# Kernel optimization log

Measured on AMD Instinct MI355X. Metric: run time of the kernel, lower is better.

## Reference

```python
import jax, jax.numpy as jnp
import numpy as np

N = 2048
D = 512
E = 65536
THR = 0.0          # config['edge_threshold']
CLUSTER_RANGE = 2
NEG_SLOPE = 0.01   # F.leaky_relu default


def segment_softmax(x, seg, num_segments):
    # torch_geometric.utils.softmax over segments (here: source nodes)
    m = jax.ops.segment_max(x, seg, num_segments)
    e = jnp.exp(x - m[seg])
    s = jax.ops.segment_sum(e, seg, num_segments)
    return e / (s[seg] + 1e-16)


def setup_inputs() -> dict:
    key = jax.random.key(0)
    k1, k2, k3 = jax.random.split(key, 3)
    embedding = jax.random.normal(k1, (N, D), dtype=jnp.float32)
    edge_index = jax.random.randint(k2, (2, E), 0, N)
    src, dst = edge_index[0], edge_index[1]
    edge_matrix = jnp.zeros((N, N), jnp.float32).at[src, dst].set(1.0)
    edge_matrix_weight = edge_matrix  # unit edge weights
    W_score = (jax.random.normal(k3, (2 * D, 1), dtype=jnp.float32) / np.sqrt(2.0 * D)).astype(jnp.float32)
    b_score = jnp.zeros((1,), jnp.float32)
    return {"embedding": embedding, "edge_index": edge_index,
            "edge_matrix": edge_matrix, "edge_matrix_weight": edge_matrix_weight,
            "W_score": W_score, "b_score": b_score}


def reference(embedding, edge_index, edge_matrix, edge_matrix_weight, W_score, b_score):
    n = embedding.shape[0]
    dt = embedding.dtype
    diag = jnp.eye(n, dtype=bool)

    # connectivity fitness: Z @ Z.T with L2-normalized rows
    Z = embedding / jnp.maximum(jnp.linalg.norm(embedding, axis=-1, keepdims=True), 1e-12)
    connectivity_M = Z @ Z.T                                   # [N,N]

    # structural fitness: edge-score -> leaky_relu -> segment softmax -> dense scatter
    src, dst = edge_index[0], edge_index[1]
    x_pair = jnp.concatenate([embedding[src], embedding[dst]], axis=-1) @ W_score + b_score  # [E,1]
    x_score = jax.nn.leaky_relu(x_pair[:, 0], NEG_SLOPE)
    x_score = segment_softmax(x_score, src, n)
    structure_M = jnp.zeros((n, n), dt).at[src, dst].add(x_score)
    fitness = connectivity_M + structure_M                     # fitness_mode == 'both_j'

    # Generate_clusters (cluster_range = 2)
    mat = jnp.where(diag, 0.0, edge_matrix)
    mat = jnp.where(fitness < THR, 0.0, mat)
    A1 = mat
    A2 = (jnp.where(diag, 0.0, A1 @ A1) > 0.5).astype(dt)
    A2 = jnp.maximum(A2 - A1, 0.0)
    cluster_matrix = ((A1 + A2) > 0).astype(dt)

    # Cluster_assignment: mean fitness per cluster matrix, nan -> 0
    scores = jnp.zeros((n,), dt)
    for A in (A1, A2):
        deg = A.sum(-1)
        scores = scores + jnp.where(deg > 0, (fitness * A).sum(-1) / jnp.where(deg > 0, deg, 1.0), 0.0)
    cluster_scores = scores / CLUSTER_RANGE

    # Select_clusters (overlap=True, pick_all=True): local extrema over A1 neighborhood
    local_extrema = (cluster_scores[:, None] - A1 * cluster_scores[None, :]) > 0
    is_cluster = local_extrema.all(axis=-1)                    # boolean cluster-center mask

    # Generate_assignment_matrix (mask-based instead of column slicing; removed
    # 'reduced' columns are kept as zero columns so shapes stay static)
    S = cluster_matrix
    S_f = cluster_matrix * fitness
    reduced = (S * is_cluster.astype(dt)[None, :]).sum(-1) > 0   # member of a selected cluster
    isolated = S.sum(0) == 0
    reduced = reduced | isolated
    keeping = (~is_cluster) & (~reduced)

    S = jnp.where(keeping[None, :], 0.0, S)
    S_f = jnp.where(keeping[None, :], 0.0, S_f)
    S = jnp.where(diag, 1.0, S)
    S_f = jnp.where(diag, 1.0, S_f)
    col_keep = (~reduced).astype(dt)[None, :]
    S = S * col_keep
    S_f = S_f * col_keep

    # pooling_mode == 'mean': pooled embedding = S_w.T @ X
    pooled = S_f.T @ embedding                                  # [N, D], zero rows = removed nodes
    return pooled
```

## Files before the change

kernel.cpp:

```cpp
#include <hip/hip_runtime.h>
#include <cstdint>
#include <cstddef>

typedef unsigned long long u64;
typedef unsigned int u32;
typedef _Float16 half8 __attribute__((ext_vector_type(8)));
typedef float f32x4 __attribute__((ext_vector_type(4)));

#define NN 2048
#define DD 512
#define EE 65536
#define NW 32

__global__ __launch_bounds__(256) void k_node(const float* __restrict__ emb,
                                              const float* __restrict__ Wsc,
                                              float* inv_norm, float* av, float* cv,
                                              _Float16* __restrict__ zh,
                                              _Float16* __restrict__ zl,
                                              float* ssum,
                                              u64* centerBits, u64* colAny, u64* EBw) {
    int n = blockIdx.x;
    int t = threadIdx.x;
    if (n < 256) EBw[n * 256 + t] = 0ull;
    else if (n < 264) { int idx = (n - 256) * 256 + t; ssum[idx] = 0.0f; }
    else if (n == 264 && t < NW) { centerBits[t] = 0ull; colAny[t] = 0ull; }

    const float* row = emb + (size_t)n * DD;
    float ss = 0.f, aa = 0.f, cc = 0.f;
    for (int d = t; d < DD; d += 256) {
        float v = row[d];
        ss += v * v;
        aa += v * Wsc[d];
        cc += v * Wsc[DD + d];
    }
    for (int off = 32; off; off >>= 1) {
        ss += __shfl_down(ss, off);
        aa += __shfl_down(aa, off);
        cc += __shfl_down(cc, off);
    }
    __shared__ float red[3][4];
    __shared__ float s_inv;
    int wid = t >> 6, lane = t & 63;
    if (lane == 0) { red[0][wid] = ss; red[1][wid] = aa; red[2][wid] = cc; }
    __syncthreads();
    if (t == 0) {
        float s = 0.f, a = 0.f, c = 0.f;
        for (int w = 0; w < 4; w++) { s += red[0][w]; a += red[1][w]; c += red[2][w]; }
        float iv = 1.0f / fmaxf(sqrtf(s), 1e-12f);
        inv_norm[n] = iv;
        s_inv = iv;
        av[n] = a;
        cv[n] = c;
    }
    __syncthreads();
    float iv = s_inv;
    for (int d = t; d < DD; d += 256) {
        float z = row[d] * iv;
        _Float16 h = (_Float16)z;
        _Float16 l = (_Float16)(z - (float)h);
        zh[(size_t)n * DD + d] = h;
        zl[(size_t)n * DD + d] = l;
    }
}

__device__ __forceinline__ float edge_score(const int* ei, const float* av, const float* cv,
                                            float b0, int e, int* src, int* dst) {
    int s = ei[e], d = ei[EE + e];
    *src = s; *dst = d;
    float x = av[s] + cv[d] + b0;
    return x > 0.f ? x : 0.01f * x;
}

__global__ __launch_bounds__(256) void k_edgeA(const int* __restrict__ ei,
                                               const float* __restrict__ av,
                                               const float* __restrict__ cv,
                                               const float* __restrict__ bsc,
                                               float* ssum, u64* EBw) {
    int e = blockIdx.x * 256 + threadIdx.x;
    if (e >= EE) return;
    int s, d;
    float x = edge_score(ei, av, cv, bsc[0], e, &s, &d);
    atomicAdd(&ssum[s], expf(x));
    atomicOr(&EBw[(size_t)s * NW + (d >> 6)], 1ull << (d & 63));
}

__global__ __launch_bounds__(256) void k_edge_scatter(const int* __restrict__ ei,
                                                      const float* __restrict__ av,
                                                      const float* __restrict__ cv,
                                                      const float* __restrict__ bsc,
                                                      const float* __restrict__ ssum,
                                                      float* fit) {
    int e = blockIdx.x * 256 + threadIdx.x;
    if (e >= EE) return;
    int s, d;
    float x = edge_score(ei, av, cv, bsc[0], e, &s, &d);
    float w = expf(x) / (ssum[s] + 1e-16f);
    atomicAdd(&fit[(size_t)s * NN + d], w);
}

#define BK 64
__global__ __launch_bounds__(256) void k_fitness(const _Float16* __restrict__ zh,
                                                 const _Float16* __restrict__ zl,
                                                 float* __restrict__ fit) {
    __shared__ _Float16 SM[4 * 64 * BK];
    _Float16* Ah = SM;
    _Float16* Al = SM + 64 * BK;
    _Float16* Bh = SM + 2 * 64 * BK;
    _Float16* Bl = SM + 3 * 64 * BK;
    int tid = threadIdx.x;
    int wid = tid >> 6, lane = tid & 63;
    int wr = wid >> 1, wc = wid & 1;
    int p = blockIdx.x, bi = 0;
    while (p >= 32 - bi) { p -= 32 - bi; bi++; }
    int bj = bi + p;
    int I = bi * 64, J = bj * 64;
    int lr = lane & 15;
    int q = lane >> 4;
    f32x4 acc[2][2] = {};

    int rl0 = tid >> 3, sl0 = tid & 7;
    int rl1 = (256 + tid) >> 3, sl1 = tid & 7;
    int ks0 = ((sl0 ^ (rl0 & 7)) << 3);
    int ks1 = ((sl1 ^ (rl1 & 7)) << 3);
    size_t gA0 = (size_t)(I + rl0) * DD + ks0, gB0 = (size_t)(J + rl0) * DD + ks0;
    size_t gA1 = (size_t)(I + rl1) * DD + ks1, gB1 = (size_t)(J + rl1) * DD + ks1;
    int lo0 = rl0 * BK + sl0 * 8, lo1 = rl1 * BK + sl1 * 8;

    {
        half8 a0 = *reinterpret_cast<const half8*>(&zh[gA0]);
        half8 a1 = *reinterpret_cast<const half8*>(&zh[gA1]);
        half8 l0 = *reinterpret_cast<const half8*>(&zl[gA0]);
        half8 l1 = *reinterpret_cast<const half8*>(&zl[gA1]);
        half8 b0 = *reinterpret_cast<const half8*>(&zh[gB0]);
        half8 b1 = *reinterpret_cast<const half8*>(&zh[gB1]);
        half8 m0 = *reinterpret_cast<const half8*>(&zl[gB0]);
        half8 m1 = *reinterpret_cast<const half8*>(&zl[gB1]);
        *reinterpret_cast<half8*>(&Ah[lo0]) = a0;
        *reinterpret_cast<half8*>(&Ah[lo1]) = a1;
        *reinterpret_cast<half8*>(&Al[lo0]) = l0;
        *reinterpret_cast<half8*>(&Al[lo1]) = l1;
        *reinterpret_cast<half8*>(&Bh[lo0]) = b0;
        *reinterpret_cast<half8*>(&Bh[lo1]) = b1;
        *reinterpret_cast<half8*>(&Bl[lo0]) = m0;
        *reinterpret_cast<half8*>(&Bl[lo1]) = m1;
    }
    __syncthreads();

    for (int k0 = 0; k0 < DD; k0 += BK) {
        half8 nA0, nA1, nAl0, nAl1, nB0, nB1, nBl0, nBl1;
        bool hasNext = (k0 + BK) < DD;
        if (hasNext) {
            int kn = k0 + BK;
            nA0  = *reinterpret_cast<const half8*>(&zh[gA0 + kn]);
            nA1  = *reinterpret_cast<const half8*>(&zh[gA1 + kn]);
            nAl0 = *reinterpret_cast<const half8*>(&zl[gA0 + kn]);
            nAl1 = *reinterpret_cast<const half8*>(&zl[gA1 + kn]);
            nB0  = *reinterpret_cast<const half8*>(&zh[gB0 + kn]);
            nB1  = *reinterpret_cast<const half8*>(&zh[gB1 + kn]);
            nBl0 = *reinterpret_cast<const half8*>(&zl[gB0 + kn]);
            nBl1 = *reinterpret_cast<const half8*>(&zl[gB1 + kn]);
        }
#pragma unroll
        for (int kk = 0; kk < 2; kk++) {
            half8 a_h[2], a_l[2], b_h[2], b_l[2];
#pragma unroll
            for (int f = 0; f < 2; f++) {
                int ra = wr * 32 + f * 16 + lr;
                int ca = (kk * 4 + q) ^ (ra & 7);
                int oa = ra * BK + ca * 8;
                a_h[f] = *reinterpret_cast<const half8*>(&Ah[oa]);
                a_l[f] = *reinterpret_cast<const half8*>(&Al[oa]);
                int rb = wc * 32 + f * 16 + lr;
                int cb = (kk * 4 + q) ^ (rb & 7);
                int ob = rb * BK + cb * 8;
                b_h[f] = *reinterpret_cast<const half8*>(&Bh[ob]);
                b_l[f] = *reinterpret_cast<const half8*>(&Bl[ob]);
            }
#pragma unroll
            for (int u = 0; u < 2; u++)
#pragma unroll
                for (int v = 0; v < 2; v++) {
                    acc[u][v] = __builtin_amdgcn_mfma_f32_16x16x32_f16(a_h[u], b_h[v], acc[u][v], 0, 0, 0);
                    acc[u][v] = __builtin_amdgcn_mfma_f32_16x16x32_f16(a_h[u], b_l[v], acc[u][v], 0, 0, 0);
                    acc[u][v] = __builtin_amdgcn_mfma_f32_16x16x32_f16(a_l[u], b_h[v], acc[u][v], 0, 0, 0);
                }
        }
        if (hasNext) {
            __syncthreads();
            *reinterpret_cast<half8*>(&Ah[lo0]) = nA0;
            *reinterpret_cast<half8*>(&Ah[lo1]) = nA1;
            *reinterpret_cast<half8*>(&Al[lo0]) = nAl0;
            *reinterpret_cast<half8*>(&Al[lo1]) = nAl1;
            *reinterpret_cast<half8*>(&Bh[lo0]) = nB0;
            *reinterpret_cast<half8*>(&Bh[lo1]) = nB1;
            *reinterpret_cast<half8*>(&Bl[lo0]) = nBl0;
            *reinterpret_cast<half8*>(&Bl[lo1]) = nBl1;
            __syncthreads();
        }
    }
#pragma unroll
    for (int u = 0; u < 2; u++) {
        int r = I + wr * 32 + u * 16 + q * 4;
#pragma unroll
        for (int v = 0; v < 2; v++) {
            int c = J + wc * 32 + v * 16 + lr;
#pragma unroll
            for (int i2 = 0; i2 < 4; i2++)
                fit[(size_t)(r + i2) * NN + c] = acc[u][v][i2];
        }
    }
    if (bi != bj) {
        __syncthreads();
        float* Tw = reinterpret_cast<float*>(SM) + wid * 528;
#pragma unroll
        for (int v = 0; v < 2; v++) {
#pragma unroll
            for (int u = 0; u < 2; u++)
#pragma unroll
                for (int i2 = 0; i2 < 4; i2++)
                    Tw[lr * 33 + u * 16 + q * 4 + i2] = acc[u][v][i2];
            int cbase = J + wc * 32 + v * 16;
            int rbase = I + wr * 32;
#pragma unroll
            for (int rr = 0; rr < 8; rr++) {
                int row = rr * 2 + (lane >> 5);
                int col = lane & 31;
                fit[(size_t)(cbase + row) * NN + rbase + col] = Tw[row * 33 + col];
            }
        }
    }
}

__global__ void k_bits(const u64* __restrict__ EBw, const float* __restrict__ fit,
                       u64* __restrict__ A1w) {
    int i = blockIdx.x;
    int t = threadIdx.x;
    int lane = t & 63, wv = t >> 6;
    for (int q = 0; q < 8; q++) {
        int j = q * 256 + t;
        u64 eb = EBw[(size_t)i * NW + (j >> 6)];
        float f = fit[(size_t)i * NN + j];
        bool pred = ((eb >> (j & 63)) & 1) && (j != i) && (f >= 0.f);
        u64 word = __ballot(pred);
        if (lane == 0) A1w[i * NW + q * 4 + wv] = word;
    }
}

__global__ __launch_bounds__(256) void k_paths2s(const u64* __restrict__ A1w,
                                                 const float* __restrict__ fit,
                                                 u64* __restrict__ A2w, u64* __restrict__ CLw,
                                                 float* cs) {
    int i = blockIdx.x;
    __shared__ u64 rowA[NW];
    __shared__ u64 rowA2[NW];
    __shared__ u64 part[8][NW];
    int t = threadIdx.x;
    if (t < NW) rowA[t] = A1w[i * NW + t];
    __syncthreads();
    int g = t >> 5, w = t & 31;
    u64 acc = 0;
    for (int ww = 0; ww < 4; ww++) {
        u64 bits = rowA[g * 4 + ww];
        int kbase = (g * 4 + ww) * 64;
        while (bits) {
            int k = __ffsll((unsigned long long)bits) - 1;
            bits &= bits - 1;
            acc |= A1w[(size_t)(kbase + k) * NW + w];
        }
    }
    part[g][w] = acc;
    __syncthreads();
    if (g == 0) {
        u64 p2 = part[0][w];
#pragma unroll
        for (int gg = 1; gg < 8; gg++) p2 |= part[gg][w];
        if ((i >> 6) == w) p2 &= ~(1ull << (i & 63));
        u64 a1 = rowA[w];
        u64 a2 = p2 & ~a1;
        u64 cl = a1 | a2;
        A2w[i * NW + w] = a2;
        CLw[i * NW + w] = cl;
        rowA2[w] = a2;
    }
    __syncthreads();
    float s1 = 0.f, s2 = 0.f;
    int d1 = 0, d2 = 0;
    for (int q = 0; q < 8; q++) {
        int j = q * 256 + t;
        float f = fit[(size_t)i * NN + j];
        int ww = j >> 6, b = j & 63;
        u64 a1 = rowA[ww], a2 = rowA2[ww];
        if ((a1 >> b) & 1) { s1 += f; d1++; }
        if ((a2 >> b) & 1) { s2 += f; d2++; }
    }
    for (int off = 32; off; off >>= 1) {
        s1 += __shfl_down(s1, off);
        s2 += __shfl_down(s2, off);
        d1 += __shfl_down(d1, off);
        d2 += __shfl_down(d2, off);
    }
    __shared__ float rs1[4], rs2[4];
    __shared__ int rd1[4], rd2[4];
    int wid = t >> 6, lane = t & 63;
    if (lane == 0) { rs1[wid] = s1; rs2[wid] = s2; rd1[wid] = d1; rd2[wid] = d2; }
    __syncthreads();
    if (t == 0) {
        float S1 = 0.f, S2 = 0.f; int D1 = 0, D2 = 0;
        for (int w2 = 0; w2 < 4; w2++) { S1 += rs1[w2]; S2 += rs2[w2]; D1 += rd1[w2]; D2 += rd2[w2]; }
        float v1 = D1 > 0 ? S1 / (float)D1 : 0.f;
        float v2 = D2 > 0 ? S2 / (float)D2 : 0.f;
        cs[i] = 0.5f * (v1 + v2);
    }
}

__global__ __launch_bounds__(256) void k_extcol(const u64* __restrict__ A1w,
                                                const u64* __restrict__ CLw,
                                                const float* __restrict__ cs,
                                                unsigned char* is_c, u64* centerBits,
                                                u64* colAny) {
    int i = blockIdx.x, t = threadIdx.x;
    __shared__ u64 part[8][NW];
    if (i < 64) {
        int sub = t >> 5, w = t & 31;
        u64 acc = 0;
#pragma unroll
        for (int k = 0; k < 4; k++) {
            int r = i * 32 + sub + k * 8;
            acc |= CLw[(size_t)r * NW + w];
        }
        part[sub][w] = acc;
    }
    float ci = cs[i];
    int ok = 1;
    for (int q = 0; q < 8; q++) {
        int j = q * 256 + t;
        u64 a1 = A1w[i * NW + (j >> 6)];
        float other = ((a1 >> (j & 63)) & 1) ? cs[j] : 0.0f;
        ok &= ((ci - other) > 0.0f) ? 1 : 0;
    }
    int all = __syncthreads_and(ok);
    if (t == 0) {
        is_c[i] = (unsigned char)(all ? 1 : 0);
        if (all) atomicOr(&centerBits[i >> 6], 1ull << (i & 63));
    }
    if (i < 64 && t < NW) {
        u64 v = part[0][t];
#pragma unroll
        for (int s = 1; s < 8; s++) v |= part[s][t];
        atomicOr(&colAny[t], v);
    }
}

__global__ __launch_bounds__(256) void k_pooled(const float* __restrict__ fit,
                                                const float* __restrict__ emb,
                                                const u64* __restrict__ CLw,
                                                const u64* __restrict__ centerBits,
                                                const u64* __restrict__ colAny,
                                                const unsigned char* __restrict__ is_c,
                                                float* __restrict__ out) {
    int j = blockIdx.x;
    int t = threadIdx.x;
    bool red = ((colAny[j >> 6] >> (j & 63)) & 1ull) == 0ull;
    for (int w = 0; w < NW; w++) red |= (CLw[(size_t)j * NW + w] & centerBits[w]) != 0ull;
    const float2* embj = reinterpret_cast<const float2*>(emb + (size_t)j * DD);
    float2* outj = reinterpret_cast<float2*>(out + (size_t)j * DD);
    bool active = is_c[j] && !red;
    if (!active) {
        float dg = red ? 0.0f : 1.0f;
        float2 v = embj[t];
        float2 o; o.x = v.x * dg; o.y = v.y * dg;
        outj[t] = o;
        return;
    }
    __shared__ int lidx[NN];
    __shared__ float lwt[NN];
    __shared__ int wcnt[4];
    int wid = t >> 6, lane = t & 63;
    int wsh = j >> 6;
    u64 bmask = 1ull << (j & 63);
    int total = 0;
    for (int qq = 0; qq < 8; qq++) {
        int i = qq * 256 + t;
        u64 cw = CLw[(size_t)i * NW + wsh];
        bool p = (cw & bmask) != 0ull;
        float f = 0.f;
        if (p) f = fit[(size_t)i * NN + j];
        u64 mask = __ballot(p);
        if (lane == 0) wcnt[wid] = __popcll(mask);
        __syncthreads();
        int off = total;
        for (int w = 0; w < wid; w++) off += wcnt[w];
        int tq = wcnt[0] + wcnt[1] + wcnt[2] + wcnt[3];
        if (p) {
            int pos = off + __popcll(mask & ((1ull << lane) - 1ull));
            lidx[pos] = i;
            lwt[pos] = f;
        }
        total += tq;
        __syncthreads();
    }
    float2 acc = {0.f, 0.f};
    int k = 0;
    for (; k + 16 <= total; k += 16) {
        int idxr[16];
        float wtr[16];
#pragma unroll
        for (int u = 0; u < 16; u++) { idxr[u] = lidx[k + u]; wtr[u] = lwt[k + u]; }
        float2 e[16];
#pragma unroll
        for (int u = 0; u < 16; u++)
            e[u] = reinterpret_cast<const float2*>(emb + (size_t)idxr[u] * DD)[t];
#pragma unroll
        for (int u = 0; u < 16; u++) {
            acc.x += wtr[u] * e[u].x;
            acc.y += wtr[u] * e[u].y;
        }
    }
    for (; k < total; k++) {
        int i = lidx[k];
        float w = lwt[k];
        float2 e = reinterpret_cast<const float2*>(emb + (size_t)i * DD)[t];
        acc.x += w * e.x;
        acc.y += w * e.y;
    }
    float2 v = embj[t];
    acc.x += v.x;
    acc.y += v.y;
    outj[t] = acc;
}

extern "C" void kernel_launch(void* const* d_in, const int* in_sizes, int n_in,
                              void* d_out, int out_size, void* d_ws, size_t ws_size,
                              hipStream_t stream) {
    const float* emb = (const float*)d_in[0];
    const int*   ei  = (const int*)d_in[1];
    const float* Wsc = (const float*)d_in[4];
    const float* bsc = (const float*)d_in[5];
    float* out = (float*)d_out;

    char* ws = (char*)d_ws;
    size_t off = 0;
    auto alloc = [&](size_t bytes) -> char* {
        char* p = ws + off;
        off = (off + bytes + 255) & ~(size_t)255;
        return p;
    };
    float* fit  = (float*)alloc((size_t)NN * NN * 4);
    char*  zblk = alloc((size_t)2 * NN * DD * 2);
    _Float16* zh = (_Float16*)zblk;
    _Float16* zl = (_Float16*)(zblk + (size_t)NN * DD * 2);
    u64* A1w = (u64*)zblk;
    u64* A2w = (u64*)(zblk + (size_t)NN * NW * 8);
    u64* CLw = (u64*)(zblk + (size_t)2 * NN * NW * 8);
    u64*   EBw        = (u64*)alloc((size_t)NN * NW * 8);
    u64*   centerBits = (u64*)alloc(NW * 8);
    u64*   colAny     = (u64*)alloc(NW * 8);
    float* inv_norm   = (float*)alloc(NN * 4);
    float* av         = (float*)alloc(NN * 4);
    float* cv         = (float*)alloc(NN * 4);
    float* ssum       = (float*)alloc(NN * 4);
    float* cs         = (float*)alloc(NN * 4);
    unsigned char* is_c = (unsigned char*)alloc(NN);

    k_node<<<dim3(NN), dim3(256), 0, stream>>>(emb, Wsc, inv_norm, av, cv, zh, zl,
                                               ssum, centerBits, colAny, EBw);
    k_edgeA<<<dim3(EE / 256), dim3(256), 0, stream>>>(ei, av, cv, bsc, ssum, EBw);
    k_fitness<<<dim3(528), dim3(256), 0, stream>>>(zh, zl, fit);
    k_edge_scatter<<<dim3(EE / 256), dim3(256), 0, stream>>>(ei, av, cv, bsc, ssum, fit);
    k_bits<<<dim3(NN), dim3(256), 0, stream>>>(EBw, fit, A1w);
    k_paths2s<<<dim3(NN), dim3(256), 0, stream>>>(A1w, fit, A2w, CLw, cs);
    k_extcol<<<dim3(NN), dim3(256), 0, stream>>>(A1w, CLw, cs, is_c, centerBits, colAny);
    k_pooled<<<dim3(NN), dim3(256), 0, stream>>>(fit, emb, CLw, centerBits, colAny, is_c, out);
}
```

Before: 146.2 us.

## Fuse all pipeline stages into one cooperative persistent kernel with grid syncs

Replaces the eight separate kernel launches with a single cooperative kernel that walks through each stage using grid-stride loops and separates dependent stages with grid.sync(). The workspace is also re-laid out so zh/zl no longer alias the bit matrices. The aim is to remove per-launch overhead and the idle gaps between small dependent kernels. In exchange, the grid is capped at 1024 blocks, so parallelism in the node and pooling stages drops, grid-wide barriers add their own cost, and occupancy is limited by the 32KB shared buffer and launch bounds.

```diff
diff --git a/kernel.cpp b/kernel.cpp
--- a/kernel.cpp
+++ b/kernel.cpp
@@ -1,6 +1,9 @@
 #include <hip/hip_runtime.h>
+#include <hip/hip_cooperative_groups.h>
 #include <cstdint>
 #include <cstddef>
+
+namespace cg = cooperative_groups;
 
 typedef unsigned long long u64;
 typedef unsigned int u32;
@@ -11,422 +14,364 @@
 #define DD 512
 #define EE 65536
 #define NW 32
-
-__global__ __launch_bounds__(256) void k_node(const float* __restrict__ emb,
-                                              const float* __restrict__ Wsc,
-                                              float* inv_norm, float* av, float* cv,
-                                              _Float16* __restrict__ zh,
-                                              _Float16* __restrict__ zl,
-                                              float* ssum,
-                                              u64* centerBits, u64* colAny, u64* EBw) {
-    int n = blockIdx.x;
-    int t = threadIdx.x;
-    if (n < 256) EBw[n * 256 + t] = 0ull;
-    else if (n < 264) { int idx = (n - 256) * 256 + t; ssum[idx] = 0.0f; }
-    else if (n == 264 && t < NW) { centerBits[t] = 0ull; colAny[t] = 0ull; }
-
-    const float* row = emb + (size_t)n * DD;
-    float ss = 0.f, aa = 0.f, cc = 0.f;
-    for (int d = t; d < DD; d += 256) {
-        float v = row[d];
-        ss += v * v;
-        aa += v * Wsc[d];
-        cc += v * Wsc[DD + d];
-    }
-    for (int off = 32; off; off >>= 1) {
-        ss += __shfl_down(ss, off);
-        aa += __shfl_down(aa, off);
-        cc += __shfl_down(cc, off);
-    }
-    __shared__ float red[3][4];
-    __shared__ float s_inv;
-    int wid = t >> 6, lane = t & 63;
-    if (lane == 0) { red[0][wid] = ss; red[1][wid] = aa; red[2][wid] = cc; }
-    __syncthreads();
-    if (t == 0) {
-        float s = 0.f, a = 0.f, c = 0.f;
-        for (int w = 0; w < 4; w++) { s += red[0][w]; a += red[1][w]; c += red[2][w]; }
-        float iv = 1.0f / fmaxf(sqrtf(s), 1e-12f);
-        inv_norm[n] = iv;
-        s_inv = iv;
-        av[n] = a;
-        cv[n] = c;
-    }
-    __syncthreads();
-    float iv = s_inv;
-    for (int d = t; d < DD; d += 256) {
-        float z = row[d] * iv;
-        _Float16 h = (_Float16)z;
-        _Float16 l = (_Float16)(z - (float)h);
-        zh[(size_t)n * DD + d] = h;
-        zl[(size_t)n * DD + d] = l;
-    }
-}
-
-__device__ __forceinline__ float edge_score(const int* ei, const float* av, const float* cv,
-                                            float b0, int e, int* src, int* dst) {
-    int s = ei[e], d = ei[EE + e];
-    *src = s; *dst = d;
-    float x = av[s] + cv[d] + b0;
-    return x > 0.f ? x : 0.01f * x;
-}
-
-__global__ __launch_bounds__(256) void k_edgeA(const int* __restrict__ ei,
-                                               const float* __restrict__ av,
-                                               const float* __restrict__ cv,
-                                               const float* __restrict__ bsc,
-                                               float* ssum, u64* EBw) {
-    int e = blockIdx.x * 256 + threadIdx.x;
-    if (e >= EE) return;
-    int s, d;
-    float x = edge_score(ei, av, cv, bsc[0], e, &s, &d);
-    atomicAdd(&ssum[s], expf(x));
-    atomicOr(&EBw[(size_t)s * NW + (d >> 6)], 1ull << (d & 63));
-}
-
-__global__ __launch_bounds__(256) void k_edge_scatter(const int* __restrict__ ei,
-                                                      const float* __restrict__ av,
-                                                      const float* __restrict__ cv,
-                                                      const float* __restrict__ bsc,
-                                                      const float* __restrict__ ssum,
-                                                      float* fit) {
-    int e = blockIdx.x * 256 + threadIdx.x;
-    if (e >= EE) return;
-    int s, d;
-    float x = edge_score(ei, av, cv, bsc[0], e, &s, &d);
-    float w = expf(x) / (ssum[s] + 1e-16f);
-    atomicAdd(&fit[(size_t)s * NN + d], w);
-}
-
 #define BK 64
-__global__ __launch_bounds__(256) void k_fitness(const _Float16* __restrict__ zh,
-                                                 const _Float16* __restrict__ zl,
-                                                 float* __restrict__ fit) {
-    __shared__ _Float16 SM[4 * 64 * BK];
-    _Float16* Ah = SM;
-    _Float16* Al = SM + 64 * BK;
-    _Float16* Bh = SM + 2 * 64 * BK;
-    _Float16* Bl = SM + 3 * 64 * BK;
-    int tid = threadIdx.x;
-    int wid = tid >> 6, lane = tid & 63;
-    int wr = wid >> 1, wc = wid & 1;
-    int p = blockIdx.x, bi = 0;
-    while (p >= 32 - bi) { p -= 32 - bi; bi++; }
-    int bj = bi + p;
-    int I = bi * 64, J = bj * 64;
-    int lr = lane & 15;
-    int q = lane >> 4;
-    f32x4 acc[2][2] = {};
-
-    int rl0 = tid >> 3, sl0 = tid & 7;
-    int rl1 = (256 + tid) >> 3, sl1 = tid & 7;
-    int ks0 = ((sl0 ^ (rl0 & 7)) << 3);
-    int ks1 = ((sl1 ^ (rl1 & 7)) << 3);
-    size_t gA0 = (size_t)(I + rl0) * DD + ks0, gB0 = (size_t)(J + rl0) * DD + ks0;
-    size_t gA1 = (size_t)(I + rl1) * DD + ks1, gB1 = (size_t)(J + rl1) * DD + ks1;
-    int lo0 = rl0 * BK + sl0 * 8, lo1 = rl1 * BK + sl1 * 8;
-
-    {
-        half8 a0 = *reinterpret_cast<const half8*>(&zh[gA0]);
-        half8 a1 = *reinterpret_cast<const half8*>(&zh[gA1]);
-        half8 l0 = *reinterpret_cast<const half8*>(&zl[gA0]);
-        half8 l1 = *reinterpret_cast<const half8*>(&zl[gA1]);
-        half8 b0 = *reinterpret_cast<const half8*>(&zh[gB0]);
-        half8 b1 = *reinterpret_cast<const half8*>(&zh[gB1]);
-        half8 m0 = *reinterpret_cast<const half8*>(&zl[gB0]);
-        half8 m1 = *reinterpret_cast<const half8*>(&zl[gB1]);
-        *reinterpret_cast<half8*>(&Ah[lo0]) = a0;
-        *reinterpret_cast<half8*>(&Ah[lo1]) = a1;
-        *reinterpret_cast<half8*>(&Al[lo0]) = l0;
-        *reinterpret_cast<half8*>(&Al[lo1]) = l1;
-        *reinterpret_cast<half8*>(&Bh[lo0]) = b0;
-        *reinterpret_cast<half8*>(&Bh[lo1]) = b1;
-        *reinterpret_cast<half8*>(&Bl[lo0]) = m0;
-        *reinterpret_cast<half8*>(&Bl[lo1]) = m1;
-    }
-    __syncthreads();
-
-    for (int k0 = 0; k0 < DD; k0 += BK) {
-        half8 nA0, nA1, nAl0, nAl1, nB0, nB1, nBl0, nBl1;
-        bool hasNext = (k0 + BK) < DD;
-        if (hasNext) {
-            int kn = k0 + BK;
-            nA0  = *reinterpret_cast<const half8*>(&zh[gA0 + kn]);
-            nA1  = *reinterpret_cast<const half8*>(&zh[gA1 + kn]);
-            nAl0 = *reinterpret_cast<const half8*>(&zl[gA0 + kn]);
-            nAl1 = *reinterpret_cast<const half8*>(&zl[gA1 + kn]);
-            nB0  = *reinterpret_cast<const half8*>(&zh[gB0 + kn]);
-            nB1  = *reinterpret_cast<const half8*>(&zh[gB1 + kn]);
-            nBl0 = *reinterpret_cast<const half8*>(&zl[gB0 + kn]);
-            nBl1 = *reinterpret_cast<const half8*>(&zl[gB1 + kn]);
-        }
-#pragma unroll
-        for (int kk = 0; kk < 2; kk++) {
-            half8 a_h[2], a_l[2], b_h[2], b_l[2];
-#pragma unroll
-            for (int f = 0; f < 2; f++) {
-                int ra = wr * 32 + f * 16 + lr;
-                int ca = (kk * 4 + q) ^ (ra & 7);
-                int oa = ra * BK + ca * 8;
-                a_h[f] = *reinterpret_cast<const half8*>(&Ah[oa]);
-                a_l[f] = *reinterpret_cast<const half8*>(&Al[oa]);
-                int rb = wc * 32 + f * 16 + lr;
-                int cb = (kk * 4 + q) ^ (rb & 7);
-                int ob = rb * BK + cb * 8;
-                b_h[f] = *reinterpret_cast<const half8*>(&Bh[ob]);
-                b_l[f] = *reinterpret_cast<const half8*>(&Bl[ob]);
-            }
-#pragma unroll
-            for (int u = 0; u < 2; u++)
+
+__device__ __forceinline__ float leaky(float x) { return x > 0.f ? x : 0.01f * x; }
+
+__global__ __launch_bounds__(256, 4) void k_mega(
+    const float* __restrict__ emb, const int* __restrict__ ei,
+    const float* __restrict__ Wsc, const float* __restrict__ bsc,
+    float* __restrict__ out,
+    float* __restrict__ fit, _Float16* __restrict__ zh, _Float16* __restrict__ zl,
+    u64* __restrict__ A1w, u64* __restrict__ A2w, u64* __restrict__ CLw,
+    u64* __restrict__ EBw, u64* centerBits, u64* colAny,
+    float* ssum, float* cs, float* av, float* cv, unsigned char* is_c)
+{
+    cg::grid_group grid = cg::this_grid();
+    __shared__ alignas(16) char SMEM[32768];
+    const int b = blockIdx.x, t = threadIdx.x, G = gridDim.x;
+    const int wid = t >> 6, lane = t & 63;
+
+    for (int idx = b * 256 + t; idx < NN * NW; idx += G * 256) EBw[idx] = 0ull;
+    for (int idx = b * 256 + t; idx < NN; idx += G * 256) ssum[idx] = 0.f;
+    if (b == 0 && t < NW) { centerBits[t] = 0ull; colAny[t] = 0ull; }
+    {
+        float* red = (float*)SMEM;
+        float* s_inv = (float*)(SMEM + 64);
+        for (int n = b; n < NN; n += G) {
+            const float* row = emb + (size_t)n * DD;
+            float ss = 0.f, aa = 0.f, cc = 0.f;
+            for (int d = t; d < DD; d += 256) {
+                float v = row[d];
+                ss += v * v; aa += v * Wsc[d]; cc += v * Wsc[DD + d];
+            }
+            for (int off = 32; off; off >>= 1) {
+                ss += __shfl_down(ss, off);
+                aa += __shfl_down(aa, off);
+                cc += __shfl_down(cc, off);
+            }
+            if (lane == 0) { red[wid] = ss; red[4 + wid] = aa; red[8 + wid] = cc; }
+            __syncthreads();
+            if (t == 0) {
+                float s = 0, a = 0, c = 0;
+                for (int w = 0; w < 4; w++) { s += red[w]; a += red[4 + w]; c += red[8 + w]; }
+                *s_inv = 1.0f / fmaxf(sqrtf(s), 1e-12f);
+                av[n] = a; cv[n] = c;
+            }
+            __syncthreads();
+            float iv = *s_inv;
+            for (int d = t; d < DD; d += 256) {
+                float z = row[d] * iv;
+                _Float16 h = (_Float16)z;
+                _Float16 l = (_Float16)(z - (float)h);
+                zh[(size_t)n * DD + d] = h;
+                zl[(size_t)n * DD + d] = l;
+            }
+            __syncthreads();
+        }
+    }
+    grid.sync();
+
+    {
+        _Float16* Ah = (_Float16*)SMEM;
+        _Float16* Al = Ah + 64 * BK;
+        _Float16* Bh = Ah + 2 * 64 * BK;
+        _Float16* Bl = Ah + 3 * 64 * BK;
+        int wr = wid >> 1, wc = wid & 1;
+        int lr = lane & 15, q = lane >> 4;
+        int rl0 = t >> 3, sl0 = t & 7;
+        int rl1 = (256 + t) >> 3, sl1 = t & 7;
+        int ks0 = ((sl0 ^ (rl0 & 7)) << 3);
+        int ks1 = ((sl1 ^ (rl1 & 7)) << 3);
+        int lo0 = rl0 * BK + sl0 * 8, lo1 = rl1 * BK + sl1 * 8;
+        for (int p0 = b; p0 < 528; p0 += G) {
+            __syncthreads();
+            int p = p0, bi = 0;
+            while (p >= 32 - bi) { p -= 32 - bi; bi++; }
+            int bj = bi + p;
+            int I = bi * 64, J = bj * 64;
+            f32x4 acc[2][2] = {};
+            size_t gA0 = (size_t)(I + rl0) * DD + ks0, gB0 = (size_t)(J + rl0) * DD + ks0;
+            size_t gA1 = (size_t)(I + rl1) * DD + ks1, gB1 = (size_t)(J + rl1) * DD + ks1;
+            {
+                half8 a0 = *(const half8*)&zh[gA0], a1 = *(const half8*)&zh[gA1];
+                half8 l0 = *(const half8*)&zl[gA0], l1 = *(const half8*)&zl[gA1];
+                half8 b0 = *(const half8*)&zh[gB0], b1 = *(const half8*)&zh[gB1];
+                half8 m0 = *(const half8*)&zl[gB0], m1 = *(const half8*)&zl[gB1];
+                *(half8*)&Ah[lo0] = a0; *(half8*)&Ah[lo1] = a1;
+                *(half8*)&Al[lo0] = l0; *(half8*)&Al[lo1] = l1;
+                *(half8*)&Bh[lo0] = b0; *(half8*)&Bh[lo1] = b1;
+                *(half8*)&Bl[lo0] = m0; *(half8*)&Bl[lo1] = m1;
+            }
+            __syncthreads();
+            for (int k0 = 0; k0 < DD; k0 += BK) {
+                half8 nA0, nA1, nAl0, nAl1, nB0, nB1, nBl0, nBl1;
+                bool hasNext = (k0 + BK) < DD;
+                if (hasNext) {
+                    int kn = k0 + BK;
+                    nA0 = *(const half8*)&zh[gA0 + kn]; nA1 = *(const half8*)&zh[gA1 + kn];
+                    nAl0 = *(const half8*)&zl[gA0 + kn]; nAl1 = *(const half8*)&zl[gA1 + kn];
+                    nB0 = *(const half8*)&zh[gB0 + kn]; nB1 = *(const half8*)&zh[gB1 + kn];
+                    nBl0 = *(const half8*)&zl[gB0 + kn]; nBl1 = *(const half8*)&zl[gB1 + kn];
+                }
+#pragma unroll
+                for (int kk = 0; kk < 2; kk++) {
+                    half8 a_h[2], a_l[2], b_h[2], b_l[2];
+#pragma unroll
+                    for (int f = 0; f < 2; f++) {
+                        int ra = wr * 32 + f * 16 + lr;
+                        int ca = (kk * 4 + q) ^ (ra & 7);
+                        a_h[f] = *(const half8*)&Ah[ra * BK + ca * 8];
+                        a_l[f] = *(const half8*)&Al[ra * BK + ca * 8];
+                        int rb = wc * 32 + f * 16 + lr;
+                        int cb = (kk * 4 + q) ^ (rb & 7);
+                        b_h[f] = *(const half8*)&Bh[rb * BK + cb * 8];
+                        b_l[f] = *(const half8*)&Bl[rb * BK + cb * 8];
+                    }
+#pragma unroll
+                    for (int u = 0; u < 2; u++)
+#pragma unroll
+                        for (int v = 0; v < 2; v++) {
+                            acc[u][v] = __builtin_amdgcn_mfma_f32_16x16x32_f16(a_h[u], b_h[v], acc[u][v], 0, 0, 0);
+                            acc[u][v] = __builtin_amdgcn_mfma_f32_16x16x32_f16(a_h[u], b_l[v], acc[u][v], 0, 0, 0);
+                            acc[u][v] = __builtin_amdgcn_mfma_f32_16x16x32_f16(a_l[u], b_h[v], acc[u][v], 0, 0, 0);
+                        }
+                }
+                if (hasNext) {
+                    __syncthreads();
+                    *(half8*)&Ah[lo0] = nA0; *(half8*)&Ah[lo1] = nA1;
+                    *(half8*)&Al[lo0] = nAl0; *(half8*)&Al[lo1] = nAl1;
+                    *(half8*)&Bh[lo0] = nB0; *(half8*)&Bh[lo1] = nB1;
+                    *(half8*)&Bl[lo0] = nBl0; *(half8*)&Bl[lo1] = nBl1;
+                    __syncthreads();
+                }
+            }
+#pragma unroll
+            for (int u = 0; u < 2; u++) {
+                int r = I + wr * 32 + u * 16 + q * 4;
 #pragma unroll
                 for (int v = 0; v < 2; v++) {
-                    acc[u][v] = __builtin_amdgcn_mfma_f32_16x16x32_f16(a_h[u], b_h[v], acc[u][v], 0, 0, 0);
-                    acc[u][v] = __builtin_amdgcn_mfma_f32_16x16x32_f16(a_h[u], b_l[v], acc[u][v], 0, 0, 0);
-                    acc[u][v] = __builtin_amdgcn_mfma_f32_16x16x32_f16(a_l[u], b_h[v], acc[u][v], 0, 0, 0);
-                }
-        }
-        if (hasNext) {
-            __syncthreads();
-            *reinterpret_cast<half8*>(&Ah[lo0]) = nA0;
-            *reinterpret_cast<half8*>(&Ah[lo1]) = nA1;
-            *reinterpret_cast<half8*>(&Al[lo0]) = nAl0;
-            *reinterpret_cast<half8*>(&Al[lo1]) = nAl1;
-            *reinterpret_cast<half8*>(&Bh[lo0]) = nB0;
-            *reinterpret_cast<half8*>(&Bh[lo1]) = nB1;
-            *reinterpret_cast<half8*>(&Bl[lo0]) = nBl0;
-            *reinterpret_cast<half8*>(&Bl[lo1]) = nBl1;
-            __syncthreads();
-        }
-    }
-#pragma unroll
-    for (int u = 0; u < 2; u++) {
-        int r = I + wr * 32 + u * 16 + q * 4;
-#pragma unroll
-        for (int v = 0; v < 2; v++) {
-            int c = J + wc * 32 + v * 16 + lr;
-#pragma unroll
-            for (int i2 = 0; i2 < 4; i2++)
-                fit[(size_t)(r + i2) * NN + c] = acc[u][v][i2];
-        }
-    }
-    if (bi != bj) {
-        __syncthreads();
-        float* Tw = reinterpret_cast<float*>(SM) + wid * 528;
-#pragma unroll
-        for (int v = 0; v < 2; v++) {
-#pragma unroll
-            for (int u = 0; u < 2; u++)
-#pragma unroll
-                for (int i2 = 0; i2 < 4; i2++)
-                    Tw[lr * 33 + u * 16 + q * 4 + i2] = acc[u][v][i2];
-            int cbase = J + wc * 32 + v * 16;
-            int rbase = I + wr * 32;
-#pragma unroll
-            for (int rr = 0; rr < 8; rr++) {
-                int row = rr * 2 + (lane >> 5);
-                int col = lane & 31;
-                fit[(size_t)(cbase + row) * NN + rbase + col] = Tw[row * 33 + col];
-            }
-        }
-    }
-}
-
-__global__ void k_bits(const u64* __restrict__ EBw, const float* __restrict__ fit,
-                       u64* __restrict__ A1w) {
-    int i = blockIdx.x;
-    int t = threadIdx.x;
-    int lane = t & 63, wv = t >> 6;
-    for (int q = 0; q < 8; q++) {
-        int j = q * 256 + t;
-        u64 eb = EBw[(size_t)i * NW + (j >> 6)];
-        float f = fit[(size_t)i * NN + j];
-        bool pred = ((eb >> (j & 63)) & 1) && (j != i) && (f >= 0.f);
-        u64 word = __ballot(pred);
-        if (lane == 0) A1w[i * NW + q * 4 + wv] = word;
-    }
-}
-
-__global__ __launch_bounds__(256) void k_paths2s(const u64* __restrict__ A1w,
-                                                 const float* __restrict__ fit,
-                                                 u64* __restrict__ A2w, u64* __restrict__ CLw,
-                                                 float* cs) {
-    int i = blockIdx.x;
-    __shared__ u64 rowA[NW];
-    __shared__ u64 rowA2[NW];
-    __shared__ u64 part[8][NW];
-    int t = threadIdx.x;
-    if (t < NW) rowA[t] = A1w[i * NW + t];
-    __syncthreads();
-    int g = t >> 5, w = t & 31;
-    u64 acc = 0;
-    for (int ww = 0; ww < 4; ww++) {
-        u64 bits = rowA[g * 4 + ww];
-        int kbase = (g * 4 + ww) * 64;
-        while (bits) {
-            int k = __ffsll((unsigned long long)bits) - 1;
-            bits &= bits - 1;
-            acc |= A1w[(size_t)(kbase + k) * NW + w];
-        }
-    }
-    part[g][w] = acc;
-    __syncthreads();
-    if (g == 0) {
-        u64 p2 = part[0][w];
-#pragma unroll
-        for (int gg = 1; gg < 8; gg++) p2 |= part[gg][w];
-        if ((i >> 6) == w) p2 &= ~(1ull << (i & 63));
-        u64 a1 = rowA[w];
-        u64 a2 = p2 & ~a1;
-        u64 cl = a1 | a2;
-        A2w[i * NW + w] = a2;
-        CLw[i * NW + w] = cl;
-        rowA2[w] = a2;
-    }
-    __syncthreads();
-    float s1 = 0.f, s2 = 0.f;
-    int d1 = 0, d2 = 0;
-    for (int q = 0; q < 8; q++) {
-        int j = q * 256 + t;
-        float f = fit[(size_t)i * NN + j];
-        int ww = j >> 6, b = j & 63;
-        u64 a1 = rowA[ww], a2 = rowA2[ww];
-        if ((a1 >> b) & 1) { s1 += f; d1++; }
-        if ((a2 >> b) & 1) { s2 += f; d2++; }
-    }
-    for (int off = 32; off; off >>= 1) {
-        s1 += __shfl_down(s1, off);
-        s2 += __shfl_down(s2, off);
-        d1 += __shfl_down(d1, off);
-        d2 += __shfl_down(d2, off);
-    }
-    __shared__ float rs1[4], rs2[4];
-    __shared__ int rd1[4], rd2[4];
-    int wid = t >> 6, lane = t & 63;
-    if (lane == 0) { rs1[wid] = s1; rs2[wid] = s2; rd1[wid] = d1; rd2[wid] = d2; }
-    __syncthreads();
-    if (t == 0) {
-        float S1 = 0.f, S2 = 0.f; int D1 = 0, D2 = 0;
-        for (int w2 = 0; w2 < 4; w2++) { S1 += rs1[w2]; S2 += rs2[w2]; D1 += rd1[w2]; D2 += rd2[w2]; }
-        float v1 = D1 > 0 ? S1 / (float)D1 : 0.f;
-        float v2 = D2 > 0 ? S2 / (float)D2 : 0.f;
-        cs[i] = 0.5f * (v1 + v2);
-    }
-}
-
-__global__ __launch_bounds__(256) void k_extcol(const u64* __restrict__ A1w,
-                                                const u64* __restrict__ CLw,
-                                                const float* __restrict__ cs,
-                                                unsigned char* is_c, u64* centerBits,
-                                                u64* colAny) {
-    int i = blockIdx.x, t = threadIdx.x;
-    __shared__ u64 part[8][NW];
-    if (i < 64) {
-        int sub = t >> 5, w = t & 31;
-        u64 acc = 0;
-#pragma unroll
-        for (int k = 0; k < 4; k++) {
-            int r = i * 32 + sub + k * 8;
-            acc |= CLw[(size_t)r * NW + w];
-        }
-        part[sub][w] = acc;
-    }
-    float ci = cs[i];
-    int ok = 1;
-    for (int q = 0; q < 8; q++) {
-        int j = q * 256 + t;
-        u64 a1 = A1w[i * NW + (j >> 6)];
-        float other = ((a1 >> (j & 63)) & 1) ? cs[j] : 0.0f;
-        ok &= ((ci - other) > 0.0f) ? 1 : 0;
-    }
-    int all = __syncthreads_and(ok);
-    if (t == 0) {
-        is_c[i] = (unsigned char)(all ? 1 : 0);
-        if (all) atomicOr(&centerBits[i >> 6], 1ull << (i & 63));
-    }
-    if (i < 64 && t < NW) {
-        u64 v = part[0][t];
-#pragma unroll
-        for (int s = 1; s < 8; s++) v |= part[s][t];
-        atomicOr(&colAny[t], v);
-    }
-}
-
-__global__ __launch_bounds__(256) void k_pooled(const float* __restrict__ fit,
-                                                const float* __restrict__ emb,
-                                                const u64* __restrict__ CLw,
-                                                const u64* __restrict__ centerBits,
-                                                const u64* __restrict__ colAny,
-                                                const unsigned char* __restrict__ is_c,
-                                                float* __restrict__ out) {
-    int j = blockIdx.x;
-    int t = threadIdx.x;
-    bool red = ((colAny[j >> 6] >> (j & 63)) & 1ull) == 0ull;
-    for (int w = 0; w < NW; w++) red |= (CLw[(size_t)j * NW + w] & centerBits[w]) != 0ull;
-    const float2* embj = reinterpret_cast<const float2*>(emb + (size_t)j * DD);
-    float2* outj = reinterpret_cast<float2*>(out + (size_t)j * DD);
-    bool active = is_c[j] && !red;
-    if (!active) {
-        float dg = red ? 0.0f : 1.0f;
-        float2 v = embj[t];
-        float2 o; o.x = v.x * dg; o.y = v.y * dg;
-        outj[t] = o;
-        return;
-    }
-    __shared__ int lidx[NN];
-    __shared__ float lwt[NN];
-    __shared__ int wcnt[4];
-    int wid = t >> 6, lane = t & 63;
-    int wsh = j >> 6;
-    u64 bmask = 1ull << (j & 63);
-    int total = 0;
-    for (int qq = 0; qq < 8; qq++) {
-        int i = qq * 256 + t;
-        u64 cw = CLw[(size_t)i * NW + wsh];
-        bool p = (cw & bmask) != 0ull;
-        float f = 0.f;
-        if (p) f = fit[(size_t)i * NN + j];
-        u64 mask = __ballot(p);
-        if (lane == 0) wcnt[wid] = __popcll(mask);
-        __syncthreads();
-        int off = total;
-        for (int w = 0; w < wid; w++) off += wcnt[w];
-        int tq = wcnt[0] + wcnt[1] + wcnt[2] + wcnt[3];
-        if (p) {
-            int pos = off + __popcll(mask & ((1ull << lane) - 1ull));
-            lidx[pos] = i;
-            lwt[pos] = f;
-        }
-        total += tq;
-        __syncthreads();
-    }
-    float2 acc = {0.f, 0.f};
-    int k = 0;
-    for (; k + 16 <= total; k += 16) {
-        int idxr[16];
-        float wtr[16];
-#pragma unroll
-        for (int u = 0; u < 16; u++) { idxr[u] = lidx[k + u]; wtr[u] = lwt[k + u]; }
-        float2 e[16];
-#pragma unroll
-        for (int u = 0; u < 16; u++)
-            e[u] = reinterpret_cast<const float2*>(emb + (size_t)idxr[u] * DD)[t];
-#pragma unroll
-        for (int u = 0; u < 16; u++) {
-            acc.x += wtr[u] * e[u].x;
-            acc.y += wtr[u] * e[u].y;
-        }
-    }
-    for (; k < total; k++) {
-        int i = lidx[k];
-        float w = lwt[k];
-        float2 e = reinterpret_cast<const float2*>(emb + (size_t)i * DD)[t];
-        acc.x += w * e.x;
-        acc.y += w * e.y;
-    }
-    float2 v = embj[t];
-    acc.x += v.x;
-    acc.y += v.y;
-    outj[t] = acc;
+                    int c = J + wc * 32 + v * 16 + lr;
+#pragma unroll
+                    for (int i2 = 0; i2 < 4; i2++)
+                        fit[(size_t)(r + i2) * NN + c] = acc[u][v][i2];
+                }
+            }
+            if (bi != bj) {
+                __syncthreads();
+                float* Tw = (float*)SMEM + wid * 528;
+#pragma unroll
+                for (int v = 0; v < 2; v++) {
+#pragma unroll
+                    for (int u = 0; u < 2; u++)
+#pragma unroll
+                        for (int i2 = 0; i2 < 4; i2++)
+                            Tw[lr * 33 + u * 16 + q * 4 + i2] = acc[u][v][i2];
+                    int cbase = J + wc * 32 + v * 16;
+                    int rbase = I + wr * 32;
+#pragma unroll
+                    for (int rr = 0; rr < 8; rr++) {
+                        int row = rr * 2 + (lane >> 5);
+                        int col = lane & 31;
+                        fit[(size_t)(cbase + row) * NN + rbase + col] = Tw[row * 33 + col];
+                    }
+                }
+            }
+        }
+        int eb = (G - 1) - b;
+        float b0v = bsc[0];
+        for (int e = eb * 256 + t; e < EE && e >= 0; e += G * 256) {
+            int s = ei[e], d = ei[EE + e];
+            float x = leaky(av[s] + cv[d] + b0v);
+            atomicAdd(&ssum[s], expf(x));
+            atomicOr(&EBw[(size_t)s * NW + (d >> 6)], 1ull << (d & 63));
+        }
+    }
+    grid.sync();
+
+    {
+        float b0v = bsc[0];
+        for (int e = b * 256 + t; e < EE; e += G * 256) {
+            int s = ei[e], d = ei[EE + e];
+            float x = leaky(av[s] + cv[d] + b0v);
+            float w = expf(x) / (ssum[s] + 1e-16f);
+            atomicAdd(&fit[(size_t)s * NN + d], w);
+        }
+    }
+    grid.sync();
+
+    for (int i = b; i < NN; i += G) {
+        int wv = t >> 6;
+        for (int qq = 0; qq < 8; qq++) {
+            int j = qq * 256 + t;
+            u64 ebv = EBw[(size_t)i * NW + (j >> 6)];
+            float f = fit[(size_t)i * NN + j];
+            bool pred = ((ebv >> (j & 63)) & 1) && (j != i) && (f >= 0.f);
+            u64 word = __ballot(pred);
+            if (lane == 0) A1w[i * NW + qq * 4 + wv] = word;
+        }
+    }
+    grid.sync();
+
+    {
+        u64* rowA = (u64*)SMEM;
+        u64* rowA2 = rowA + NW;
+        u64* part = rowA2 + NW;
+        float* rs1 = (float*)(part + 8 * NW);
+        float* rs2 = rs1 + 4;
+        int* rd1 = (int*)(rs2 + 4);
+        int* rd2 = rd1 + 4;
+        for (int i = b; i < NN; i += G) {
+            __syncthreads();
+            if (t < NW) rowA[t] = A1w[i * NW + t];
+            __syncthreads();
+            int g = t >> 5, w = t & 31;
+            u64 acc = 0;
+            for (int ww = 0; ww < 4; ww++) {
+                u64 bits = rowA[g * 4 + ww];
+                int kbase = (g * 4 + ww) * 64;
+                while (bits) {
+                    int k = __ffsll((unsigned long long)bits) - 1;
+                    bits &= bits - 1;
+                    acc |= A1w[(size_t)(kbase + k) * NW + w];
+                }
+            }
+            part[g * NW + w] = acc;
+            __syncthreads();
+            if (g == 0) {
+                u64 p2 = part[w];
+#pragma unroll
+                for (int gg = 1; gg < 8; gg++) p2 |= part[gg * NW + w];
+                if ((i >> 6) == w) p2 &= ~(1ull << (i & 63));
+                u64 a1 = rowA[w];
+                u64 a2 = p2 & ~a1;
+                A2w[i * NW + w] = a2;
+                CLw[i * NW + w] = a1 | a2;
+                rowA2[w] = a2;
+            }
+            __syncthreads();
+            float s1 = 0, s2 = 0; int d1 = 0, d2 = 0;
+            for (int qq = 0; qq < 8; qq++) {
+                int j = qq * 256 + t;
+                float f = fit[(size_t)i * NN + j];
+                int ww = j >> 6, bb = j & 63;
+                if ((rowA[ww] >> bb) & 1) { s1 += f; d1++; }
+                if ((rowA2[ww] >> bb) & 1) { s2 += f; d2++; }
+            }
+            for (int off = 32; off; off >>= 1) {
+                s1 += __shfl_down(s1, off); s2 += __shfl_down(s2, off);
+                d1 += __shfl_down(d1, off); d2 += __shfl_down(d2, off);
+            }
+            if (lane == 0) { rs1[wid] = s1; rs2[wid] = s2; rd1[wid] = d1; rd2[wid] = d2; }
+            __syncthreads();
+            if (t == 0) {
+                float S1 = 0, S2 = 0; int D1 = 0, D2 = 0;
+                for (int w2 = 0; w2 < 4; w2++) { S1 += rs1[w2]; S2 += rs2[w2]; D1 += rd1[w2]; D2 += rd2[w2]; }
+                float v1 = D1 > 0 ? S1 / (float)D1 : 0.f;
+                float v2 = D2 > 0 ? S2 / (float)D2 : 0.f;
+                cs[i] = 0.5f * (v1 + v2);
+            }
+        }
+    }
+    grid.sync();
+
+    for (int i = b; i < NN; i += G) {
+        float ci = cs[i];
+        int ok = 1;
+        for (int qq = 0; qq < 8; qq++) {
+            int j = qq * 256 + t;
+            u64 a1 = A1w[i * NW + (j >> 6)];
+            float other = ((a1 >> (j & 63)) & 1) ? cs[j] : 0.0f;
+            ok &= ((ci - other) > 0.0f) ? 1 : 0;
+        }
+        int all = __syncthreads_and(ok);
+        if (t == 0) {
+            is_c[i] = (unsigned char)(all ? 1 : 0);
+            if (all) atomicOr(&centerBits[i >> 6], 1ull << (i & 63));
+        }
+    }
+    {
+        u64* part = (u64*)SMEM;
+        for (int cb2 = b; cb2 < 64; cb2 += G) {
+            __syncthreads();
+            int sub = t >> 5, w = t & 31;
+            u64 acc = 0;
+#pragma unroll
+            for (int k = 0; k < 4; k++) acc |= CLw[(size_t)(cb2 * 32 + sub + k * 8) * NW + w];
+            part[sub * NW + w] = acc;
+            __syncthreads();
+            if (t < NW) {
+                u64 v = part[t];
+#pragma unroll
+                for (int s2 = 1; s2 < 8; s2++) v |= part[s2 * NW + t];
+                atomicOr(&colAny[t], v);
+            }
+        }
+    }
+    grid.sync();
+
+    {
+        int* lidx = (int*)SMEM;
+        float* lwt = (float*)(SMEM + NN * 4);
+        int* wcnt = (int*)(SMEM + NN * 8);
+        for (int j = b; j < NN; j += G) {
+            __syncthreads();
+            bool red = ((colAny[j >> 6] >> (j & 63)) & 1ull) == 0ull;
+            for (int w = 0; w < NW; w++) red |= (CLw[(size_t)j * NW + w] & centerBits[w]) != 0ull;
+            const float2* embj = (const float2*)(emb + (size_t)j * DD);
+            float2* outj = (float2*)(out + (size_t)j * DD);
+            bool active = is_c[j] && !red;
+            if (!active) {
+                float dg = red ? 0.f : 1.f;
+                float2 v = embj[t];
+                float2 o; o.x = v.x * dg; o.y = v.y * dg;
+                outj[t] = o;
+                continue;
+            }
+            int wsh = j >> 6;
+            u64 bmask = 1ull << (j & 63);
+            int total = 0;
+            for (int qq = 0; qq < 8; qq++) {
+                int i = qq * 256 + t;
+                u64 cw = CLw[(size_t)i * NW + wsh];
+                bool pp = (cw & bmask) != 0ull;
+                float f = 0.f;
+                if (pp) f = fit[(size_t)i * NN + j];
+                u64 mask = __ballot(pp);
+                if (lane == 0) wcnt[wid] = __popcll(mask);
+                __syncthreads();
+                int off = total;
+                for (int w = 0; w < wid; w++) off += wcnt[w];
+                int tq = wcnt[0] + wcnt[1] + wcnt[2] + wcnt[3];
+                if (pp) {
+                    int pos = off + __popcll(mask & ((1ull << lane) - 1ull));
+                    lidx[pos] = i; lwt[pos] = f;
+                }
+                total += tq;
+                __syncthreads();
+            }
+            float2 acc = {0.f, 0.f};
+            int k = 0;
+            for (; k + 16 <= total; k += 16) {
+                int idxr[16]; float wtr[16];
+#pragma unroll
+                for (int u = 0; u < 16; u++) { idxr[u] = lidx[k + u]; wtr[u] = lwt[k + u]; }
+                float2 e[16];
+#pragma unroll
+                for (int u = 0; u < 16; u++) e[u] = ((const float2*)(emb + (size_t)idxr[u] * DD))[t];
+#pragma unroll
+                for (int u = 0; u < 16; u++) { acc.x += wtr[u] * e[u].x; acc.y += wtr[u] * e[u].y; }
+            }
+            for (; k < total; k++) {
+                int i = lidx[k]; float w = lwt[k];
+                float2 e = ((const float2*)(emb + (size_t)i * DD))[t];
+                acc.x += w * e.x; acc.y += w * e.y;
+            }
+            float2 v = embj[t];
+            acc.x += v.x; acc.y += v.y;
+            outj[t] = acc;
+        }
+    }
 }
 
 extern "C" void kernel_launch(void* const* d_in, const int* in_sizes, int n_in,
@@ -445,30 +390,32 @@
         off = (off + bytes + 255) & ~(size_t)255;
         return p;
     };
-    float* fit  = (float*)alloc((size_t)NN * NN * 4);
-    char*  zblk = alloc((size_t)2 * NN * DD * 2);
-    _Float16* zh = (_Float16*)zblk;
-    _Float16* zl = (_Float16*)(zblk + (size_t)NN * DD * 2);
-    u64* A1w = (u64*)zblk;
-    u64* A2w = (u64*)(zblk + (size_t)NN * NW * 8);
-    u64* CLw = (u64*)(zblk + (size_t)2 * NN * NW * 8);
-    u64*   EBw        = (u64*)alloc((size_t)NN * NW * 8);
-    u64*   centerBits = (u64*)alloc(NW * 8);
-    u64*   colAny     = (u64*)alloc(NW * 8);
-    float* inv_norm   = (float*)alloc(NN * 4);
-    float* av         = (float*)alloc(NN * 4);
-    float* cv         = (float*)alloc(NN * 4);
-    float* ssum       = (float*)alloc(NN * 4);
-    float* cs         = (float*)alloc(NN * 4);
+    float*    fit = (float*)alloc((size_t)NN * NN * 4);
+    _Float16* zh  = (_Float16*)alloc((size_t)NN * DD * 2);
+    _Float16* zl  = (_Float16*)alloc((size_t)NN * DD * 2);
+    u64* A1w = (u64*)alloc((size_t)NN * NW * 8);
+    u64* A2w = (u64*)alloc((size_t)NN * NW * 8);
+    u64* CLw = (u64*)alloc((size_t)NN * NW * 8);
+    u64* EBw = (u64*)alloc((size_t)NN * NW * 8);
+    u64* centerBits = (u64*)alloc(NW * 8);
+    u64* colAny     = (u64*)alloc(NW * 8);
+    float* ssum = (float*)alloc(NN * 4);
+    float* cs   = (float*)alloc(NN * 4);
+    float* av   = (float*)alloc(NN * 4);
+    float* cv   = (float*)alloc(NN * 4);
     unsigned char* is_c = (unsigned char*)alloc(NN);
 
-    k_node<<<dim3(NN), dim3(256), 0, stream>>>(emb, Wsc, inv_norm, av, cv, zh, zl,
-                                               ssum, centerBits, colAny, EBw);
-    k_edgeA<<<dim3(EE / 256), dim3(256), 0, stream>>>(ei, av, cv, bsc, ssum, EBw);
-    k_fitness<<<dim3(528), dim3(256), 0, stream>>>(zh, zl, fit);
-    k_edge_scatter<<<dim3(EE / 256), dim3(256), 0, stream>>>(ei, av, cv, bsc, ssum, fit);
-    k_bits<<<dim3(NN), dim3(256), 0, stream>>>(EBw, fit, A1w);
-    k_paths2s<<<dim3(NN), dim3(256), 0, stream>>>(A1w, fit, A2w, CLw, cs);
-    k_extcol<<<dim3(NN), dim3(256), 0, stream>>>(A1w, CLw, cs, is_c, centerBits, colAny);
-    k_pooled<<<dim3(NN), dim3(256), 0, stream>>>(fit, emb, CLw, centerBits, colAny, is_c, out);
+    int maxB = 0;
+    hipOccupancyMaxActiveBlocksPerMultiprocessor(&maxB, (const void*)k_mega, 256, 0);
+    int G = (maxB > 0) ? maxB * 256 : 512;
+    if (G > 1024) G = 1024;
+
+    void* args[] = {
+        (void*)&emb, (void*)&ei, (void*)&Wsc, (void*)&bsc, (void*)&out,
+        (void*)&fit, (void*)&zh, (void*)&zl,
+        (void*)&A1w, (void*)&A2w, (void*)&CLw, (void*)&EBw,
+        (void*)&centerBits, (void*)&colAny,
+        (void*)&ssum, (void*)&cs, (void*)&av, (void*)&cv, (void*)&is_c
+    };
+    hipLaunchCooperativeKernel((const void*)k_mega, dim3(G), dim3(256), args, 0, stream);
 }
```

Result: slower. 513.0 us (+250.8%).
